# Kernel optimization log

Hardware: AMD Instinct MI355X
Metric: run time of the kernel (lower is better)

## Reference

```python
import jax, jax.numpy as jnp
import numpy as np

REACH = 2
BS = 32  # blocksize
NHID = 15  # nlayers - 1
CI = 12    # 2*(reach+1)*reach


def _offsets():
    # matches get_nb ordering: rows above (dy=-2,-1; dx=-2..2), then left (dy=0; dx=-2,-1)
    offs = [(dy, dx) for dy in range(-REACH, 0) for dx in range(-REACH, REACH + 1)]
    offs += [(0, dx) for dx in range(-REACH, 0)]
    return offs


def setup_inputs() -> dict:
    key = jax.random.key(0)
    k0, k1, k2, k3, k4 = jax.random.split(key, 5)
    x = jax.random.uniform(k0, (8, 3, 512, 512), jnp.float32, -1.0, 1.0)
    s = 1.0 / np.sqrt(CI).astype(np.float32)
    Wh = jax.random.uniform(k1, (NHID, CI, CI), jnp.float32, -s, s)
    bh = jax.random.uniform(k2, (NHID, CI), jnp.float32, -s, s)
    Wo = jax.random.uniform(k3, (1, CI), jnp.float32, -s, s)
    bo = jax.random.uniform(k4, (1,), jnp.float32, -s, s)
    return {"x": x, "Wh": Wh, "bh": bh, "Wo": Wo, "bo": bo}


def reference(x, Wh, bh, Wo, bo):
    b, c, h, w = x.shape
    h = h // BS * BS
    w = w // BS * BS
    x = x[:, :, :h, :w]
    nbh, nbw = h // BS, w // BS
    # unfold into (nbc, BS, BS) blocks, matching torch unfold/unfold/reshape
    blocks = x.reshape(b, c, nbh, BS, nbw, BS).transpose(0, 1, 2, 4, 3, 5).reshape(-1, BS, BS)
    xp = jnp.pad(blocks, ((0, 0), (REACH, REACH), (REACH, REACH)))
    # batched causal-neighbor gather: (nbc, BS, BS, 12)
    feats = jnp.stack(
        [xp[:, REACH + dy:REACH + dy + BS, REACH + dx:REACH + dx + BS] for dy, dx in _offsets()],
        axis=-1,
    )
    hdn = feats
    for l in range(NHID):
        hdn = jax.nn.leaky_relu(jnp.einsum('nhwi,oi->nhwo', hdn, Wh[l]) + bh[l])
    pred = jnp.clip(jnp.einsum('nhwi,oi->nhwo', hdn, Wo)[..., 0] + bo[0], -1.0, 1.0)
    deltas = jnp.fmod(blocks - pred + 1.0, 2.0) - 1.0
    deltas = deltas.reshape(b * c, h * w)
    loss1 = 255.0 * jnp.sqrt(jnp.mean(jnp.square(deltas)))
    return (loss1, deltas)
```

## Files before the change

### kernel.cpp

```cpp
#include <hip/hip_runtime.h>
#include <math.h>

#define CI 12
#define NHID 15
#define NBLK 6144
#define NPIX (NBLK * 1024)

typedef int i32x4 __attribute__((ext_vector_type(4)));

static __device__ __forceinline__ int h2pack(float lo, float hi) {
    auto h = __builtin_amdgcn_cvt_pkrtz(lo, hi);
    int r;
    __builtin_memcpy(&r, &h, 4);
    return r;
}

#define LKA \
  "v_cvt_pkrtz_f16_f32 v36, v52, v53\n" \
  "v_cvt_pkrtz_f16_f32 v37, v54, v55\n" \
  "v_pk_mul_f16 v68, s21, v36\n" \
  "v_pk_mul_f16 v69, s21, v37\n" \
  "v_pk_max_f16 v36, v36, v68\n" \
  "v_pk_max_f16 v37, v37, v69\n"
#define LKB \
  "v_cvt_pkrtz_f16_f32 v40, v56, v57\n" \
  "v_cvt_pkrtz_f16_f32 v41, v58, v59\n" \
  "v_pk_mul_f16 v68, s21, v40\n" \
  "v_pk_mul_f16 v69, s21, v41\n" \
  "v_pk_max_f16 v40, v40, v68\n" \
  "v_pk_max_f16 v41, v41, v69\n"
#define LKC \
  "v_cvt_pkrtz_f16_f32 v44, v60, v61\n" \
  "v_cvt_pkrtz_f16_f32 v45, v62, v63\n" \
  "v_pk_mul_f16 v68, s21, v44\n" \
  "v_pk_mul_f16 v69, s21, v45\n" \
  "v_pk_max_f16 v44, v44, v68\n" \
  "v_pk_max_f16 v45, v45, v69\n"
#define LKD \
  "v_cvt_pkrtz_f16_f32 v48, v64, v65\n" \
  "v_cvt_pkrtz_f16_f32 v49, v66, v67\n" \
  "v_pk_mul_f16 v68, s21, v48\n" \
  "v_pk_mul_f16 v69, s21, v49\n" \
  "v_pk_max_f16 v48, v48, v68\n" \
  "v_pk_max_f16 v49, v49, v69\n"

#define MFA(w) "v_mfma_f32_16x16x32_f16 v[52:55], %[" w "], v[36:39], v[32:35]\n"
#define MFB(w) "v_mfma_f32_16x16x32_f16 v[56:59], %[" w "], v[40:43], v[32:35]\n"
#define MFC(w) "v_mfma_f32_16x16x32_f16 v[60:63], %[" w "], v[44:47], v[32:35]\n"
#define MFD(w) "v_mfma_f32_16x16x32_f16 v[64:67], %[" w "], v[48:51], v[32:35]\n"

#define LAYER(w) LKA LKB MFA(w) LKC MFB(w) LKD MFC(w) "s_nop 1\n" MFD(w)

__global__ __launch_bounds__(256, 3) void codec_main(
    const float* __restrict__ x,
    const float* __restrict__ Wh,
    const float* __restrict__ bh,
    const float* __restrict__ Wo,
    const float* __restrict__ bo,
    float* __restrict__ out,
    float* __restrict__ loss_acc)
{
    __shared__ float tile[36 * 37];
    __shared__ float stage[4][256];
    __shared__ float wsum[4];

    const int n    = blockIdx.x;
    const int tid  = threadIdx.x;
    const int lane = tid & 63;
    const int wv   = tid >> 6;
    const int t    = lane & 15;
    const int q    = lane >> 4;

    {
        const int col = tid & 31;
        const int r0  = tid >> 5;
        #pragma unroll
        for (int i = 0; i < 6; ++i) {
            int idx = tid + i * 256;
            if (idx < 36 * 37) tile[idx] = 0.0f;
        }
        __syncthreads();
        const int bc  = n >> 8;
        const int blk = n & 255;
        const int by  = blk >> 4;
        const int bx  = blk & 15;
        #pragma unroll
        for (int p = 0; p < 4; ++p) {
            const int row = r0 + 8 * p;
            tile[(row + 2) * 37 + col + 2] =
                x[((size_t)bc * 512 + (size_t)(by * 32 + row)) * 512
                  + (size_t)(bx * 32 + col)];
        }
        __syncthreads();
    }

    i32x4 wq[16];
    const bool wok = (t < CI) && (q < 3);
    #pragma unroll
    for (int l = 0; l < NHID; ++l) {
        float4 w = {0.f, 0.f, 0.f, 0.f};
        float  b = 0.f;
        if (wok) w = *(const float4*)(Wh + l * (CI * CI) + t * CI + 4 * q);
        if (wok && q == 0) b = bh[l * CI + t];
        wq[l] = (i32x4){ h2pack(w.x, w.y), h2pack(w.z, w.w),
                         h2pack(b, 0.f), 0 };
    }
    {
        float4 w = {0.f, 0.f, 0.f, 0.f};
        float  b = 0.f;
        if (t == 0 && q < 3) w = *(const float4*)(Wo + 4 * q);
        if (t == 0 && q == 0) b = bo[0];
        wq[15] = (i32x4){ h2pack(w.x, w.y), h2pack(w.z, w.w),
                          h2pack(b, 0.f), 0 };
    }

    const int sh8  = q * 8;
    const int off0 = (int)(signed char)((0x00DCB8B4u >> sh8) & 0xFFu);
    const int off1 = (int)(signed char)((0x00DDD9B5u >> sh8) & 0xFFu);
    const int off2 = (int)(signed char)((0x00FEDAB6u >> sh8) & 0xFFu);
    const int off3 = (int)(signed char)((0x00FFDBB7u >> sh8) & 0xFFu);

    const int biasreg = (q == 0) ? 0x00003C00 : 0;
    int e = (wv * 8 + 2) * 37 + (t + 2);

    float d2 = 0.0f;
    #pragma unroll 1
    for (int yi = 0; yi < 4; ++yi) {
        const int faA0 = h2pack(tile[e + off0],      tile[e + off1]);
        const int faA1 = h2pack(tile[e + off2],      tile[e + off3]);
        const int fbA0 = h2pack(tile[e + off0 + 16], tile[e + off1 + 16]);
        const int fbA1 = h2pack(tile[e + off2 + 16], tile[e + off3 + 16]);
        const int fcA0 = h2pack(tile[e + off0 + 37], tile[e + off1 + 37]);
        const int fcA1 = h2pack(tile[e + off2 + 37], tile[e + off3 + 37]);
        const int fdA0 = h2pack(tile[e + off0 + 53], tile[e + off1 + 53]);
        const int fdA1 = h2pack(tile[e + off2 + 53], tile[e + off3 + 53]);
        const float vA = tile[e], vB = tile[e + 16];
        const float vC = tile[e + 37], vD = tile[e + 53];

        float pA, pB, pC, pD;
        asm volatile(
            "s_mov_b32 s21, 0x211f211f\n"
            "v_mov_b32 v32, 0\n" "v_mov_b32 v33, 0\n"
            "v_mov_b32 v34, 0\n" "v_mov_b32 v35, 0\n"
            "v_mov_b32 v36, %[fa0]\n" "v_mov_b32 v37, %[fa1]\n"
            "v_mov_b32 v38, %[bias]\n" "v_mov_b32 v39, 0\n"
            "v_mov_b32 v40, %[fb0]\n" "v_mov_b32 v41, %[fb1]\n"
            "v_mov_b32 v42, %[bias]\n" "v_mov_b32 v43, 0\n"
            "v_mov_b32 v44, %[fc0]\n" "v_mov_b32 v45, %[fc1]\n"
            "v_mov_b32 v46, %[bias]\n" "v_mov_b32 v47, 0\n"
            "v_mov_b32 v48, %[fd0]\n" "v_mov_b32 v49, %[fd1]\n"
            "v_mov_b32 v50, %[bias]\n" "v_mov_b32 v51, 0\n"
            MFA("w0") MFB("w0") MFC("w0") MFD("w0")
            "s_nop 7\n" "s_nop 7\n" "s_nop 7\n"
            LAYER("w1")  LAYER("w2")  LAYER("w3")  LAYER("w4")
            LAYER("w5")  LAYER("w6")  LAYER("w7")  LAYER("w8")
            LAYER("w9")  LAYER("w10") LAYER("w11") LAYER("w12")
            LAYER("w13") LAYER("w14") LAYER("w15")
            "v_mov_b32 %[pA], v52\n"
            "s_nop 1\n"
            "v_mov_b32 %[pB], v56\n"
            "s_nop 7\n" "s_nop 7\n"
            "v_mov_b32 %[pC], v60\n"
            "s_nop 3\n"
            "v_mov_b32 %[pD], v64\n"
            : [pA] "=v"(pA), [pB] "=v"(pB), [pC] "=v"(pC), [pD] "=v"(pD)
            : [w0] "a"(wq[0]),  [w1] "a"(wq[1]),  [w2] "a"(wq[2]),
              [w3] "a"(wq[3]),  [w4] "a"(wq[4]),  [w5] "a"(wq[5]),
              [w6] "a"(wq[6]),  [w7] "a"(wq[7]),  [w8] "a"(wq[8]),
              [w9] "a"(wq[9]),  [w10] "a"(wq[10]), [w11] "a"(wq[11]),
              [w12] "a"(wq[12]), [w13] "a"(wq[13]), [w14] "a"(wq[14]),
              [w15] "a"(wq[15]),
              [fa0] "v"(faA0), [fa1] "v"(faA1), [fb0] "v"(fbA0), [fb1] "v"(fbA1),
              [fc0] "v"(fcA0), [fc1] "v"(fcA1), [fd0] "v"(fdA0), [fd1] "v"(fdA1),
              [bias] "v"(biasreg)
            : "s21",
              "v32","v33","v34","v35","v36","v37","v38","v39",
              "v40","v41","v42","v43","v44","v45","v46","v47",
              "v48","v49","v50","v51","v52","v53","v54","v55",
              "v56","v57","v58","v59","v60","v61","v62","v63",
              "v64","v65","v66","v67","v68","v69");

        if (lane < 16) {
            const float qA = fminf(fmaxf(pA, -1.0f), 1.0f);
            const float uA = vA - qA + 1.0f;
            const float dA = uA - ((uA < 2.0f) ? 1.0f : 3.0f);
            const float qB = fminf(fmaxf(pB, -1.0f), 1.0f);
            const float uB = vB - qB + 1.0f;
            const float dB = uB - ((uB < 2.0f) ? 1.0f : 3.0f);
            const float qC = fminf(fmaxf(pC, -1.0f), 1.0f);
            const float uC = vC - qC + 1.0f;
            const float dC = uC - ((uC < 2.0f) ? 1.0f : 3.0f);
            const float qD = fminf(fmaxf(pD, -1.0f), 1.0f);
            const float uD = vD - qD + 1.0f;
            const float dD = uD - ((uD < 2.0f) ? 1.0f : 3.0f);
            const int r = 2 * yi;
            stage[wv][r * 32 + t]            = dA;
            stage[wv][r * 32 + 16 + t]       = dB;
            stage[wv][(r + 1) * 32 + t]      = dC;
            stage[wv][(r + 1) * 32 + 16 + t] = dD;
            d2 = fmaf(dA, dA, fmaf(dB, dB, fmaf(dC, dC, fmaf(dD, dD, d2))));
        }
        e += 74;
    }

    float* outp = out + 1 + (size_t)n * 1024 + wv * 256;
    #pragma unroll
    for (int j = 0; j < 4; ++j)
        outp[j * 64 + lane] = stage[wv][j * 64 + lane];

    #pragma unroll
    for (int off = 8; off > 0; off >>= 1) d2 += __shfl_down(d2, off, 64);
    if (lane == 0) wsum[wv] = d2;
    __syncthreads();
    if (tid == 0) atomicAdd(loss_acc, wsum[0] + wsum[1] + wsum[2] + wsum[3]);
}

__global__ void codec_loss(const float* __restrict__ acc, float* __restrict__ out)
{
    out[0] = 255.0f * sqrtf(acc[0] / (float)NPIX);
}

extern "C" void kernel_launch(void* const* d_in, const int* in_sizes, int n_in,
                              void* d_out, int out_size, void* d_ws, size_t ws_size,
                              hipStream_t stream)
{
    const float* x  = (const float*)d_in[0];
    const float* Wh = (const float*)d_in[1];
    const float* bh = (const float*)d_in[2];
    const float* Wo = (const float*)d_in[3];
    const float* bo = (const float*)d_in[4];
    float* out = (float*)d_out;
    float* acc = (float*)d_ws;

    hipMemsetAsync(acc, 0, sizeof(float), stream);
    codec_main<<<NBLK, 256, 0, stream>>>(x, Wh, bh, Wo, bo, out, acc);
    codec_loss<<<1, 1, 0, stream>>>(acc, out);
}
```

Before: 192.0 us.

## Switch MLP MFMA from 16x16x32 to 16x16x16 with bias folded into K

Replaces the K=32 f16 MFMA with the K=16 variant. The 12 input features use K slots 0-11, and the bias is carried through a constant-one lane (q==3, t==CI), so each layer needs only 16 K elements instead of 32. This halves the weight and activation operand registers and removes the separate bias register setup. The freed registers allow raising launch bounds from 3 to 4 waves per SIMD. The per-MFMA latency is also lower, but the hand-tuned s_nop hazard padding is adjusted only partially, so dependency timing between layers could be off.

Result: faster. 183.7 us (-4.3%).

```diff
diff --git a/kernel.cpp b/kernel.cpp
--- a/kernel.cpp
+++ b/kernel.cpp
@@ -6,7 +6,7 @@
 #define NBLK 6144
 #define NPIX (NBLK * 1024)
 
-typedef int i32x4 __attribute__((ext_vector_type(4)));
+typedef int i32x2 __attribute__((ext_vector_type(2)));
 
 static __device__ __forceinline__ int h2pack(float lo, float hi) {
     auto h = __builtin_amdgcn_cvt_pkrtz(lo, hi);
@@ -16,42 +16,42 @@
 }
 
 #define LKA \
-  "v_cvt_pkrtz_f16_f32 v36, v52, v53\n" \
-  "v_cvt_pkrtz_f16_f32 v37, v54, v55\n" \
-  "v_pk_mul_f16 v68, s21, v36\n" \
-  "v_pk_mul_f16 v69, s21, v37\n" \
-  "v_pk_max_f16 v36, v36, v68\n" \
-  "v_pk_max_f16 v37, v37, v69\n"
+  "v_cvt_pkrtz_f16_f32 v36, v44, v45\n" \
+  "v_cvt_pkrtz_f16_f32 v37, v46, v47\n" \
+  "v_pk_mul_f16 v60, s21, v36\n" \
+  "v_pk_mul_f16 v61, s21, v37\n" \
+  "v_pk_max_f16 v36, v36, v60\n" \
+  "v_pk_max_f16 v37, v37, v61\n"
 #define LKB \
-  "v_cvt_pkrtz_f16_f32 v40, v56, v57\n" \
-  "v_cvt_pkrtz_f16_f32 v41, v58, v59\n" \
-  "v_pk_mul_f16 v68, s21, v40\n" \
-  "v_pk_mul_f16 v69, s21, v41\n" \
-  "v_pk_max_f16 v40, v40, v68\n" \
-  "v_pk_max_f16 v41, v41, v69\n"
+  "v_cvt_pkrtz_f16_f32 v38, v48, v49\n" \
+  "v_cvt_pkrtz_f16_f32 v39, v50, v51\n" \
+  "v_pk_mul_f16 v60, s21, v38\n" \
+  "v_pk_mul_f16 v61, s21, v39\n" \
+  "v_pk_max_f16 v38, v38, v60\n" \
+  "v_pk_max_f16 v39, v39, v61\n"
 #define LKC \
-  "v_cvt_pkrtz_f16_f32 v44, v60, v61\n" \
-  "v_cvt_pkrtz_f16_f32 v45, v62, v63\n" \
-  "v_pk_mul_f16 v68, s21, v44\n" \
-  "v_pk_mul_f16 v69, s21, v45\n" \
-  "v_pk_max_f16 v44, v44, v68\n" \
-  "v_pk_max_f16 v45, v45, v69\n"
+  "v_cvt_pkrtz_f16_f32 v40, v52, v53\n" \
+  "v_cvt_pkrtz_f16_f32 v41, v54, v55\n" \
+  "v_pk_mul_f16 v60, s21, v40\n" \
+  "v_pk_mul_f16 v61, s21, v41\n" \
+  "v_pk_max_f16 v40, v40, v60\n" \
+  "v_pk_max_f16 v41, v41, v61\n"
 #define LKD \
-  "v_cvt_pkrtz_f16_f32 v48, v64, v65\n" \
-  "v_cvt_pkrtz_f16_f32 v49, v66, v67\n" \
-  "v_pk_mul_f16 v68, s21, v48\n" \
-  "v_pk_mul_f16 v69, s21, v49\n" \
-  "v_pk_max_f16 v48, v48, v68\n" \
-  "v_pk_max_f16 v49, v49, v69\n"
-
-#define MFA(w) "v_mfma_f32_16x16x32_f16 v[52:55], %[" w "], v[36:39], v[32:35]\n"
-#define MFB(w) "v_mfma_f32_16x16x32_f16 v[56:59], %[" w "], v[40:43], v[32:35]\n"
-#define MFC(w) "v_mfma_f32_16x16x32_f16 v[60:63], %[" w "], v[44:47], v[32:35]\n"
-#define MFD(w) "v_mfma_f32_16x16x32_f16 v[64:67], %[" w "], v[48:51], v[32:35]\n"
+  "v_cvt_pkrtz_f16_f32 v42, v56, v57\n" \
+  "v_cvt_pkrtz_f16_f32 v43, v58, v59\n" \
+  "v_pk_mul_f16 v60, s21, v42\n" \
+  "v_pk_mul_f16 v61, s21, v43\n" \
+  "v_pk_max_f16 v42, v42, v60\n" \
+  "v_pk_max_f16 v43, v43, v61\n"
+
+#define MFA(w) "v_mfma_f32_16x16x16_f16 v[44:47], %[" w "], v[36:37], v[32:35]\n"
+#define MFB(w) "v_mfma_f32_16x16x16_f16 v[48:51], %[" w "], v[38:39], v[32:35]\n"
+#define MFC(w) "v_mfma_f32_16x16x16_f16 v[52:55], %[" w "], v[40:41], v[32:35]\n"
+#define MFD(w) "v_mfma_f32_16x16x16_f16 v[56:59], %[" w "], v[42:43], v[32:35]\n"
 
 #define LAYER(w) LKA LKB MFA(w) LKC MFB(w) LKD MFC(w) "s_nop 1\n" MFD(w)
 
-__global__ __launch_bounds__(256, 3) void codec_main(
+__global__ __launch_bounds__(256, 4) void codec_main(
     const float* __restrict__ x,
     const float* __restrict__ Wh,
     const float* __restrict__ bh,
@@ -94,24 +94,28 @@
         __syncthreads();
     }
 
-    i32x4 wq[16];
-    const bool wok = (t < CI) && (q < 3);
+    i32x2 wq[16];
     #pragma unroll
     for (int l = 0; l < NHID; ++l) {
-        float4 w = {0.f, 0.f, 0.f, 0.f};
-        float  b = 0.f;
-        if (wok) w = *(const float4*)(Wh + l * (CI * CI) + t * CI + 4 * q);
-        if (wok && q == 0) b = bh[l * CI + t];
-        wq[l] = (i32x4){ h2pack(w.x, w.y), h2pack(w.z, w.w),
-                         h2pack(b, 0.f), 0 };
+        int w0 = 0, w1 = 0;
+        if (q < 3 && t < CI) {
+            float4 w = *(const float4*)(Wh + l * (CI * CI) + t * CI + 4 * q);
+            w0 = h2pack(w.x, w.y);
+            w1 = h2pack(w.z, w.w);
+        }
+        if (q == 3 && t < CI)  w0 = h2pack(bh[l * CI + t], 0.f);
+        if (q == 3 && t == CI) w0 = 0x3C00;
+        wq[l] = (i32x2){ w0, w1 };
     }
     {
-        float4 w = {0.f, 0.f, 0.f, 0.f};
-        float  b = 0.f;
-        if (t == 0 && q < 3) w = *(const float4*)(Wo + 4 * q);
-        if (t == 0 && q == 0) b = bo[0];
-        wq[15] = (i32x4){ h2pack(w.x, w.y), h2pack(w.z, w.w),
-                          h2pack(b, 0.f), 0 };
+        int w0 = 0, w1 = 0;
+        if (t == 0 && q < 3) {
+            float4 w = *(const float4*)(Wo + 4 * q);
+            w0 = h2pack(w.x, w.y);
+            w1 = h2pack(w.z, w.w);
+        }
+        if (t == 0 && q == 3) w0 = h2pack(bo[0], 0.f);
+        wq[15] = (i32x2){ w0, w1 };
     }
 
     const int sh8  = q * 8;
@@ -119,21 +123,21 @@
     const int off1 = (int)(signed char)((0x00DDD9B5u >> sh8) & 0xFFu);
     const int off2 = (int)(signed char)((0x00FEDAB6u >> sh8) & 0xFFu);
     const int off3 = (int)(signed char)((0x00FFDBB7u >> sh8) & 0xFFu);
-
-    const int biasreg = (q == 0) ? 0x00003C00 : 0;
+    const bool q3  = (q == 3);
+
     int e = (wv * 8 + 2) * 37 + (t + 2);
 
     float d2 = 0.0f;
     #pragma unroll 1
     for (int yi = 0; yi < 4; ++yi) {
-        const int faA0 = h2pack(tile[e + off0],      tile[e + off1]);
-        const int faA1 = h2pack(tile[e + off2],      tile[e + off3]);
-        const int fbA0 = h2pack(tile[e + off0 + 16], tile[e + off1 + 16]);
-        const int fbA1 = h2pack(tile[e + off2 + 16], tile[e + off3 + 16]);
-        const int fcA0 = h2pack(tile[e + off0 + 37], tile[e + off1 + 37]);
-        const int fcA1 = h2pack(tile[e + off2 + 37], tile[e + off3 + 37]);
-        const int fdA0 = h2pack(tile[e + off0 + 53], tile[e + off1 + 53]);
-        const int fdA1 = h2pack(tile[e + off2 + 53], tile[e + off3 + 53]);
+        const int faA0 = q3 ? 0x3C00 : h2pack(tile[e + off0],      tile[e + off1]);
+        const int faA1 = q3 ? 0      : h2pack(tile[e + off2],      tile[e + off3]);
+        const int fbA0 = q3 ? 0x3C00 : h2pack(tile[e + off0 + 16], tile[e + off1 + 16]);
+        const int fbA1 = q3 ? 0      : h2pack(tile[e + off2 + 16], tile[e + off3 + 16]);
+        const int fcA0 = q3 ? 0x3C00 : h2pack(tile[e + off0 + 37], tile[e + off1 + 37]);
+        const int fcA1 = q3 ? 0      : h2pack(tile[e + off2 + 37], tile[e + off3 + 37]);
+        const int fdA0 = q3 ? 0x3C00 : h2pack(tile[e + off0 + 53], tile[e + off1 + 53]);
+        const int fdA1 = q3 ? 0      : h2pack(tile[e + off2 + 53], tile[e + off3 + 53]);
         const float vA = tile[e], vB = tile[e + 16];
         const float vC = tile[e + 37], vD = tile[e + 53];
 
@@ -143,26 +147,22 @@
             "v_mov_b32 v32, 0\n" "v_mov_b32 v33, 0\n"
             "v_mov_b32 v34, 0\n" "v_mov_b32 v35, 0\n"
             "v_mov_b32 v36, %[fa0]\n" "v_mov_b32 v37, %[fa1]\n"
-            "v_mov_b32 v38, %[bias]\n" "v_mov_b32 v39, 0\n"
-            "v_mov_b32 v40, %[fb0]\n" "v_mov_b32 v41, %[fb1]\n"
-            "v_mov_b32 v42, %[bias]\n" "v_mov_b32 v43, 0\n"
-            "v_mov_b32 v44, %[fc0]\n" "v_mov_b32 v45, %[fc1]\n"
-            "v_mov_b32 v46, %[bias]\n" "v_mov_b32 v47, 0\n"
-            "v_mov_b32 v48, %[fd0]\n" "v_mov_b32 v49, %[fd1]\n"
-            "v_mov_b32 v50, %[bias]\n" "v_mov_b32 v51, 0\n"
+            "v_mov_b32 v38, %[fb0]\n" "v_mov_b32 v39, %[fb1]\n"
+            "v_mov_b32 v40, %[fc0]\n" "v_mov_b32 v41, %[fc1]\n"
+            "v_mov_b32 v42, %[fd0]\n" "v_mov_b32 v43, %[fd1]\n"
             MFA("w0") MFB("w0") MFC("w0") MFD("w0")
-            "s_nop 7\n" "s_nop 7\n" "s_nop 7\n"
+            "s_nop 7\n" "s_nop 7\n" "s_nop 7\n" "s_nop 4\n"
             LAYER("w1")  LAYER("w2")  LAYER("w3")  LAYER("w4")
             LAYER("w5")  LAYER("w6")  LAYER("w7")  LAYER("w8")
             LAYER("w9")  LAYER("w10") LAYER("w11") LAYER("w12")
             LAYER("w13") LAYER("w14") LAYER("w15")
-            "v_mov_b32 %[pA], v52\n"
+            "v_mov_b32 %[pA], v44\n"
             "s_nop 1\n"
-            "v_mov_b32 %[pB], v56\n"
+            "v_mov_b32 %[pB], v48\n"
             "s_nop 7\n" "s_nop 7\n"
-            "v_mov_b32 %[pC], v60\n"
+            "v_mov_b32 %[pC], v52\n"
             "s_nop 3\n"
-            "v_mov_b32 %[pD], v64\n"
+            "v_mov_b32 %[pD], v56\n"
             : [pA] "=v"(pA), [pB] "=v"(pB), [pC] "=v"(pC), [pD] "=v"(pD)
             : [w0] "a"(wq[0]),  [w1] "a"(wq[1]),  [w2] "a"(wq[2]),
               [w3] "a"(wq[3]),  [w4] "a"(wq[4]),  [w5] "a"(wq[5]),
@@ -171,14 +171,12 @@
               [w12] "a"(wq[12]), [w13] "a"(wq[13]), [w14] "a"(wq[14]),
               [w15] "a"(wq[15]),
               [fa0] "v"(faA0), [fa1] "v"(faA1), [fb0] "v"(fbA0), [fb1] "v"(fbA1),
-              [fc0] "v"(fcA0), [fc1] "v"(fcA1), [fd0] "v"(fdA0), [fd1] "v"(fdA1),
-              [bias] "v"(biasreg)
+              [fc0] "v"(fcA0), [fc1] "v"(fcA1), [fd0] "v"(fdA0), [fd1] "v"(fdA1)
             : "s21",
               "v32","v33","v34","v35","v36","v37","v38","v39",
               "v40","v41","v42","v43","v44","v45","v46","v47",
               "v48","v49","v50","v51","v52","v53","v54","v55",
-              "v56","v57","v58","v59","v60","v61","v62","v63",
-              "v64","v65","v66","v67","v68","v69");
+              "v56","v57","v58","v59","v60","v61");
 
         if (lane < 16) {
             const float qA = fminf(fmaxf(pA, -1.0f), 1.0f);
```

## Stream MFMA weights from LDS with triple buffering to raise occupancy

Applied to the files above, without the earlier changes.

The packed per-layer fp16 weight fragments no longer sit in 64 AGPRs per thread. Wave 0 builds them once per block in a shared-memory table, and the inline-asm layer chain now loads each layer's fragment with ds_read_b128 into a rotating three-buffer set, prefetched ahead of use with lgkmcnt waits. The freed registers let launch bounds go from 3 to 5 blocks per CU, so more waves can hide the serial MFMA and activation dependency chain. In exchange, every layer adds LDS traffic and wait points, each block needs about 16KB more shared memory, and the hand-tuned waitcnt and nop schedule has to stay correct.

Measured after the change: 189.9 us. About the same (-1.1%).

```diff
diff --git a/kernel.cpp b/kernel.cpp
--- a/kernel.cpp
+++ b/kernel.cpp
@@ -15,43 +15,35 @@
     return r;
 }
 
-#define LKA \
-  "v_cvt_pkrtz_f16_f32 v36, v52, v53\n" \
-  "v_cvt_pkrtz_f16_f32 v37, v54, v55\n" \
-  "v_pk_mul_f16 v68, s21, v36\n" \
-  "v_pk_mul_f16 v69, s21, v37\n" \
-  "v_pk_max_f16 v36, v36, v68\n" \
-  "v_pk_max_f16 v37, v37, v69\n"
-#define LKB \
-  "v_cvt_pkrtz_f16_f32 v40, v56, v57\n" \
-  "v_cvt_pkrtz_f16_f32 v41, v58, v59\n" \
-  "v_pk_mul_f16 v68, s21, v40\n" \
-  "v_pk_mul_f16 v69, s21, v41\n" \
-  "v_pk_max_f16 v40, v40, v68\n" \
-  "v_pk_max_f16 v41, v41, v69\n"
-#define LKC \
-  "v_cvt_pkrtz_f16_f32 v44, v60, v61\n" \
-  "v_cvt_pkrtz_f16_f32 v45, v62, v63\n" \
-  "v_pk_mul_f16 v68, s21, v44\n" \
-  "v_pk_mul_f16 v69, s21, v45\n" \
-  "v_pk_max_f16 v44, v44, v68\n" \
-  "v_pk_max_f16 v45, v45, v69\n"
-#define LKD \
-  "v_cvt_pkrtz_f16_f32 v48, v64, v65\n" \
-  "v_cvt_pkrtz_f16_f32 v49, v66, v67\n" \
-  "v_pk_mul_f16 v68, s21, v48\n" \
-  "v_pk_mul_f16 v69, s21, v49\n" \
-  "v_pk_max_f16 v48, v48, v68\n" \
-  "v_pk_max_f16 v49, v49, v69\n"
-
-#define MFA(w) "v_mfma_f32_16x16x32_f16 v[52:55], %[" w "], v[36:39], v[32:35]\n"
-#define MFB(w) "v_mfma_f32_16x16x32_f16 v[56:59], %[" w "], v[40:43], v[32:35]\n"
-#define MFC(w) "v_mfma_f32_16x16x32_f16 v[60:63], %[" w "], v[44:47], v[32:35]\n"
-#define MFD(w) "v_mfma_f32_16x16x32_f16 v[64:67], %[" w "], v[48:51], v[32:35]\n"
-
-#define LAYER(w) LKA LKB MFA(w) LKC MFB(w) LKD MFC(w) "s_nop 1\n" MFD(w)
-
-__global__ __launch_bounds__(256, 3) void codec_main(
+#define LK4(D0,D1,D2,D3,B0,B1) \
+  "v_cvt_pkrtz_f16_f32 " B0 ", " D0 ", " D1 "\n" \
+  "v_cvt_pkrtz_f16_f32 " B1 ", " D2 ", " D3 "\n" \
+  "v_pk_mul_f16 v68, s21, " B0 "\n" \
+  "v_pk_mul_f16 v69, s21, " B1 "\n" \
+  "v_pk_max_f16 " B0 ", " B0 ", v68\n" \
+  "v_pk_max_f16 " B1 ", " B1 ", v69\n"
+
+#define LKA LK4("v52","v53","v54","v55","v36","v37")
+#define LKB LK4("v56","v57","v58","v59","v40","v41")
+#define LKC LK4("v60","v61","v62","v63","v44","v45")
+#define LKD LK4("v64","v65","v66","v67","v48","v49")
+
+#define MFA(B) "v_mfma_f32_16x16x32_f16 v[52:55], v[" B "], v[36:39], v[32:35]\n"
+#define MFB(B) "v_mfma_f32_16x16x32_f16 v[56:59], v[" B "], v[40:43], v[32:35]\n"
+#define MFC(B) "v_mfma_f32_16x16x32_f16 v[60:63], v[" B "], v[44:47], v[32:35]\n"
+#define MFD(B) "v_mfma_f32_16x16x32_f16 v[64:67], v[" B "], v[48:51], v[32:35]\n"
+
+#define BUF0 "70:73"
+#define BUF1 "74:77"
+#define BUF2 "78:81"
+
+#define RD(B, OFF) "ds_read_b128 v[" B "], %[wa] offset:" OFF "\n"
+#define W2 "s_waitcnt lgkmcnt(2)\n"
+
+#define LAYER(B, PRE, WT) \
+  PRE WT LKA LKB MFA(B) LKC MFB(B) LKD MFC(B) "s_nop 1\n" MFD(B)
+
+__global__ __launch_bounds__(256, 5) void codec_main(
     const float* __restrict__ x,
     const float* __restrict__ Wh,
     const float* __restrict__ bh,
@@ -61,6 +53,7 @@
     float* __restrict__ loss_acc)
 {
     __shared__ float tile[36 * 37];
+    __shared__ i32x4 lgw[16][64];
     __shared__ float stage[4][256];
     __shared__ float wsum[4];
 
@@ -91,27 +84,27 @@
                 x[((size_t)bc * 512 + (size_t)(by * 32 + row)) * 512
                   + (size_t)(bx * 32 + col)];
         }
+        if (wv == 0) {
+            const bool wok = (t < CI) && (q < 3);
+            #pragma unroll
+            for (int l = 0; l < NHID; ++l) {
+                float4 w = {0.f, 0.f, 0.f, 0.f};
+                float  b = 0.f;
+                if (wok) w = *(const float4*)(Wh + l * (CI * CI) + t * CI + 4 * q);
+                if (wok && q == 0) b = bh[l * CI + t];
+                lgw[l][lane] = (i32x4){ h2pack(w.x, w.y), h2pack(w.z, w.w),
+                                        h2pack(b, 0.f), 0 };
+            }
+            {
+                float4 w = {0.f, 0.f, 0.f, 0.f};
+                float  b = 0.f;
+                if (t == 0 && q < 3) w = *(const float4*)(Wo + 4 * q);
+                if (t == 0 && q == 0) b = bo[0];
+                lgw[15][lane] = (i32x4){ h2pack(w.x, w.y), h2pack(w.z, w.w),
+                                         h2pack(b, 0.f), 0 };
+            }
+        }
         __syncthreads();
-    }
-
-    i32x4 wq[16];
-    const bool wok = (t < CI) && (q < 3);
-    #pragma unroll
-    for (int l = 0; l < NHID; ++l) {
-        float4 w = {0.f, 0.f, 0.f, 0.f};
-        float  b = 0.f;
-        if (wok) w = *(const float4*)(Wh + l * (CI * CI) + t * CI + 4 * q);
-        if (wok && q == 0) b = bh[l * CI + t];
-        wq[l] = (i32x4){ h2pack(w.x, w.y), h2pack(w.z, w.w),
-                         h2pack(b, 0.f), 0 };
-    }
-    {
-        float4 w = {0.f, 0.f, 0.f, 0.f};
-        float  b = 0.f;
-        if (t == 0 && q < 3) w = *(const float4*)(Wo + 4 * q);
-        if (t == 0 && q == 0) b = bo[0];
-        wq[15] = (i32x4){ h2pack(w.x, w.y), h2pack(w.z, w.w),
-                          h2pack(b, 0.f), 0 };
     }
 
     const int sh8  = q * 8;
@@ -120,7 +113,8 @@
     const int off2 = (int)(signed char)((0x00FEDAB6u >> sh8) & 0xFFu);
     const int off3 = (int)(signed char)((0x00FFDBB7u >> sh8) & 0xFFu);
 
-    const int biasreg = (q == 0) ? 0x00003C00 : 0;
+    const unsigned waddr = (unsigned)(uintptr_t)(&lgw[0][lane]);
+
     int e = (wv * 8 + 2) * 37 + (t + 2);
 
     float d2 = 0.0f;
@@ -136,6 +130,7 @@
         const int fdA1 = h2pack(tile[e + off2 + 53], tile[e + off3 + 53]);
         const float vA = tile[e], vB = tile[e + 16];
         const float vC = tile[e + 37], vD = tile[e + 53];
+        asm volatile("" :: "v"(vA), "v"(vB), "v"(vC), "v"(vD));
 
         float pA, pB, pC, pD;
         asm volatile(
@@ -143,19 +138,32 @@
             "v_mov_b32 v32, 0\n" "v_mov_b32 v33, 0\n"
             "v_mov_b32 v34, 0\n" "v_mov_b32 v35, 0\n"
             "v_mov_b32 v36, %[fa0]\n" "v_mov_b32 v37, %[fa1]\n"
-            "v_mov_b32 v38, %[bias]\n" "v_mov_b32 v39, 0\n"
+            "v_mov_b32 v38, 0x3c00\n" "v_mov_b32 v39, 0\n"
             "v_mov_b32 v40, %[fb0]\n" "v_mov_b32 v41, %[fb1]\n"
-            "v_mov_b32 v42, %[bias]\n" "v_mov_b32 v43, 0\n"
+            "v_mov_b32 v42, 0x3c00\n" "v_mov_b32 v43, 0\n"
             "v_mov_b32 v44, %[fc0]\n" "v_mov_b32 v45, %[fc1]\n"
-            "v_mov_b32 v46, %[bias]\n" "v_mov_b32 v47, 0\n"
+            "v_mov_b32 v46, 0x3c00\n" "v_mov_b32 v47, 0\n"
             "v_mov_b32 v48, %[fd0]\n" "v_mov_b32 v49, %[fd1]\n"
-            "v_mov_b32 v50, %[bias]\n" "v_mov_b32 v51, 0\n"
-            MFA("w0") MFB("w0") MFC("w0") MFD("w0")
+            "v_mov_b32 v50, 0x3c00\n" "v_mov_b32 v51, 0\n"
+            RD(BUF0, "0") RD(BUF1, "1024") RD(BUF2, "2048")
+            W2
+            MFA(BUF0) MFB(BUF0) MFC(BUF0) MFD(BUF0)
             "s_nop 7\n" "s_nop 7\n" "s_nop 7\n"
-            LAYER("w1")  LAYER("w2")  LAYER("w3")  LAYER("w4")
-            LAYER("w5")  LAYER("w6")  LAYER("w7")  LAYER("w8")
-            LAYER("w9")  LAYER("w10") LAYER("w11") LAYER("w12")
-            LAYER("w13") LAYER("w14") LAYER("w15")
+            LAYER(BUF1, RD(BUF0, "3072"),  W2)
+            LAYER(BUF2, RD(BUF1, "4096"),  W2)
+            LAYER(BUF0, RD(BUF2, "5120"),  W2)
+            LAYER(BUF1, RD(BUF0, "6144"),  W2)
+            LAYER(BUF2, RD(BUF1, "7168"),  W2)
+            LAYER(BUF0, RD(BUF2, "8192"),  W2)
+            LAYER(BUF1, RD(BUF0, "9216"),  W2)
+            LAYER(BUF2, RD(BUF1, "10240"), W2)
+            LAYER(BUF0, RD(BUF2, "11264"), W2)
+            LAYER(BUF1, RD(BUF0, "12288"), W2)
+            LAYER(BUF2, RD(BUF1, "13312"), W2)
+            LAYER(BUF0, RD(BUF2, "14336"), W2)
+            LAYER(BUF1, RD(BUF0, "15360"), W2)
+            LAYER(BUF2, "", "s_waitcnt lgkmcnt(1)\n")
+            LAYER(BUF0, "", "s_waitcnt lgkmcnt(0)\n")
             "v_mov_b32 %[pA], v52\n"
             "s_nop 1\n"
             "v_mov_b32 %[pB], v56\n"
@@ -164,21 +172,17 @@
             "s_nop 3\n"
             "v_mov_b32 %[pD], v64\n"
             : [pA] "=v"(pA), [pB] "=v"(pB), [pC] "=v"(pC), [pD] "=v"(pD)
-            : [w0] "a"(wq[0]),  [w1] "a"(wq[1]),  [w2] "a"(wq[2]),
-              [w3] "a"(wq[3]),  [w4] "a"(wq[4]),  [w5] "a"(wq[5]),
-              [w6] "a"(wq[6]),  [w7] "a"(wq[7]),  [w8] "a"(wq[8]),
-              [w9] "a"(wq[9]),  [w10] "a"(wq[10]), [w11] "a"(wq[11]),
-              [w12] "a"(wq[12]), [w13] "a"(wq[13]), [w14] "a"(wq[14]),
-              [w15] "a"(wq[15]),
-              [fa0] "v"(faA0), [fa1] "v"(faA1), [fb0] "v"(fbA0), [fb1] "v"(fbA1),
+            : [fa0] "v"(faA0), [fa1] "v"(faA1), [fb0] "v"(fbA0), [fb1] "v"(fbA1),
               [fc0] "v"(fcA0), [fc1] "v"(fcA1), [fd0] "v"(fdA0), [fd1] "v"(fdA1),
-              [bias] "v"(biasreg)
+              [wa] "v"(waddr)
             : "s21",
               "v32","v33","v34","v35","v36","v37","v38","v39",
               "v40","v41","v42","v43","v44","v45","v46","v47",
               "v48","v49","v50","v51","v52","v53","v54","v55",
               "v56","v57","v58","v59","v60","v61","v62","v63",
-              "v64","v65","v66","v67","v68","v69");
+              "v64","v65","v66","v67","v68","v69","v70","v71",
+              "v72","v73","v74","v75","v76","v77","v78","v79",
+              "v80","v81");
 
         if (lane < 16) {
             const float qA = fminf(fmaxf(pA, -1.0f), 1.0f);
```
